# Performance work log

Measured on AMD Instinct MI355X. Metric: run time of the kernel, lower is better.

The kernel has to match this reference:

```python
import jax, jax.numpy as jnp
import numpy as np

NUM_HEADS = 16
THETA = 10000.0


def setup_inputs() -> dict:
    key = jax.random.key(0)
    ks = jax.random.split(key, 5)
    b, s, dm = 4, 2048, 2048
    sigma = np.sqrt(2.0 / (dm + dm))
    return {
        "x": jax.random.normal(ks[0], (b, s, dm), dtype=jnp.float32),
        "token_positions": jnp.arange(s, dtype=jnp.int64),
        "Wq": jax.random.normal(ks[1], (dm, dm), dtype=jnp.float32) * sigma,
        "Wk": jax.random.normal(ks[2], (dm, dm), dtype=jnp.float32) * sigma,
        "Wv": jax.random.normal(ks[3], (dm, dm), dtype=jnp.float32) * sigma,
        "Wo": jax.random.normal(ks[4], (dm, dm), dtype=jnp.float32) * sigma,
    }


def _apply_rope(x, positions):
    # x: [b, h, s, d]; positions: [s]
    d = x.shape[-1]
    half = d // 2
    inv_freq = THETA ** (-jnp.arange(half, dtype=x.dtype) / half)  # [half]
    ang = positions.astype(x.dtype)[:, None] * inv_freq           # [s, half]
    cos, sin = jnp.cos(ang), jnp.sin(ang)
    x2 = x.reshape(*x.shape[:-1], half, 2)   # even/odd interleaved pairs
    even, odd = x2[..., 0], x2[..., 1]
    rot_even = even * cos - odd * sin
    rot_odd = odd * cos + even * sin
    return jnp.stack([rot_even, rot_odd], axis=-1).reshape(x.shape)


def reference(x, token_positions, Wq, Wk, Wv, Wo):
    b, s, dm = x.shape
    h = NUM_HEADS
    d = dm // h

    def proj(W):
        return jnp.einsum('bsm,nm->bsn', x, W).reshape(b, s, h, d).transpose(0, 2, 1, 3)

    Q = _apply_rope(proj(Wq), token_positions)
    K = _apply_rope(proj(Wk), token_positions)
    V = proj(Wv)

    scores = jnp.einsum('bhqd,bhkd->bhqk', Q, K) / jnp.sqrt(jnp.asarray(d, x.dtype))
    causal = jnp.tril(jnp.ones((s, s), dtype=bool))
    scores = jnp.where(causal, scores, jnp.asarray(-jnp.inf, x.dtype))
    attn = jax.nn.softmax(scores, axis=-1)
    y = jnp.einsum('bhqk,bhkd->bhqd', attn, V)
    y = y.transpose(0, 2, 1, 3).reshape(b, s, dm)
    return jnp.einsum('bsm,nm->bsn', y, Wo)
```

## Files before the change

### kernel.cpp

```cpp
#include <hip/hip_runtime.h>
#include <hip/hip_bf16.h>
#include <math.h>

#define NUM_HEADS 16
#define HEAD_DIM  128
#define SEQ       2048
#define DM        2048
#define BATCH     4
#define M_ROWS    (BATCH * SEQ)

typedef short  short8 __attribute__((ext_vector_type(8)));
typedef float  f32x4  __attribute__((ext_vector_type(4)));

__device__ inline unsigned short f2bf(float f) {
    union { float f; unsigned u; } x; x.f = f;
    unsigned r = x.u + 0x7FFF + ((x.u >> 16) & 1);
    return (unsigned short)(r >> 16);
}

__device__ inline float bf2f(unsigned short u) {
    union { unsigned u; float f; } x; x.u = ((unsigned)u) << 16;
    return x.f;
}

__global__ __launch_bounds__(256)
void splitk(const float* __restrict__ src, unsigned short* __restrict__ dh,
            unsigned short* __restrict__ dl, int n4) {
    const int stride = gridDim.x * 256;
    for (int i = blockIdx.x * 256 + threadIdx.x; i < n4; i += stride) {
        const float4 v = ((const float4*)src)[i];
        ushort4 h, l;
        h.x = f2bf(v.x); l.x = f2bf(v.x - bf2f(h.x));
        h.y = f2bf(v.y); l.y = f2bf(v.y - bf2f(h.y));
        h.z = f2bf(v.z); l.z = f2bf(v.z - bf2f(h.z));
        h.w = f2bf(v.w); l.w = f2bf(v.w - bf2f(h.w));
        ((ushort4*)dh)[i] = h;
        ((ushort4*)dl)[i] = l;
    }
}

#define BKT  32
#define LDST 40

__global__ __launch_bounds__(256)
void mgemm2(const unsigned short* __restrict__ Ah, const unsigned short* __restrict__ Al,
            const unsigned short* __restrict__ Ag,
            const unsigned short* __restrict__ Bh, const unsigned short* __restrict__ Bl,
            unsigned short* __restrict__ Cb, float* __restrict__ Cf, int mode) {
    __shared__ __align__(16) unsigned short AsH[128 * LDST];
    __shared__ __align__(16) unsigned short AsL[128 * LDST];
    __shared__ __align__(16) unsigned short BsH[128 * LDST];
    __shared__ __align__(16) unsigned short BsL[128 * LDST];

    const int tid = threadIdx.x;
    const int lane = tid & 63, wave = tid >> 6;
    const int lo = lane & 15, hi = lane >> 4;
    const int wm = wave >> 1, wn = wave & 1;
    const int tm = blockIdx.y * 128, tn = blockIdx.x * 128;
    const bool split = (Ag == nullptr);

    const int sr = tid >> 2;
    const int sc = (tid & 3) * 8;

    f32x4 acc[4][4];
    #pragma unroll
    for (int mf = 0; mf < 4; ++mf)
        #pragma unroll
        for (int nf = 0; nf < 4; ++nf) acc[mf][nf] = (f32x4){0.f, 0.f, 0.f, 0.f};

    for (int k0 = 0; k0 < DM; k0 += BKT) {
        if (k0) __syncthreads();
        #pragma unroll
        for (int j = 0; j < 2; ++j) {
            const int r = j * 64 + sr;
            if (split) {
                *(short8*)&AsH[r * LDST + sc] =
                    *(const short8*)&Ah[(size_t)(tm + r) * DM + k0 + sc];
                *(short8*)&AsL[r * LDST + sc] =
                    *(const short8*)&Al[(size_t)(tm + r) * DM + k0 + sc];
            } else {
                const int row = tm + r;
                const int b = row >> 11, s = row & (SEQ - 1);
                const int hh = k0 >> 7, dd = (k0 & (HEAD_DIM - 1)) + sc;
                *(short8*)&AsH[r * LDST + sc] = *(const short8*)
                    &Ag[(((size_t)b * NUM_HEADS + hh) * SEQ + s) * HEAD_DIM + dd];
            }
            *(short8*)&BsH[r * LDST + sc] =
                *(const short8*)&Bh[(size_t)(tn + r) * DM + k0 + sc];
            *(short8*)&BsL[r * LDST + sc] =
                *(const short8*)&Bl[(size_t)(tn + r) * DM + k0 + sc];
        }
        __syncthreads();

        short8 a0[4], b0[4], tf[4];
        #pragma unroll
        for (int mf = 0; mf < 4; ++mf)
            a0[mf] = *(const short8*)&AsH[(wm * 64 + mf * 16 + lo) * LDST + hi * 8];
        #pragma unroll
        for (int nf = 0; nf < 4; ++nf)
            b0[nf] = *(const short8*)&BsH[(wn * 64 + nf * 16 + lo) * LDST + hi * 8];
        #pragma unroll
        for (int mf = 0; mf < 4; ++mf)
            #pragma unroll
            for (int nf = 0; nf < 4; ++nf)
                acc[mf][nf] = __builtin_amdgcn_mfma_f32_16x16x32_bf16(
                    a0[mf], b0[nf], acc[mf][nf], 0, 0, 0);
        if (split) {
            #pragma unroll
            for (int mf = 0; mf < 4; ++mf)
                tf[mf] = *(const short8*)&AsL[(wm * 64 + mf * 16 + lo) * LDST + hi * 8];
            #pragma unroll
            for (int mf = 0; mf < 4; ++mf)
                #pragma unroll
                for (int nf = 0; nf < 4; ++nf)
                    acc[mf][nf] = __builtin_amdgcn_mfma_f32_16x16x32_bf16(
                        tf[mf], b0[nf], acc[mf][nf], 0, 0, 0);
        }
        #pragma unroll
        for (int nf = 0; nf < 4; ++nf)
            tf[nf] = *(const short8*)&BsL[(wn * 64 + nf * 16 + lo) * LDST + hi * 8];
        #pragma unroll
        for (int mf = 0; mf < 4; ++mf)
            #pragma unroll
            for (int nf = 0; nf < 4; ++nf)
                acc[mf][nf] = __builtin_amdgcn_mfma_f32_16x16x32_bf16(
                    a0[mf], tf[nf], acc[mf][nf], 0, 0, 0);
    }

    const int r0 = tm + wm * 64, c0 = tn + wn * 64;
    #pragma unroll
    for (int mf = 0; mf < 4; ++mf) {
        #pragma unroll
        for (int nf = 0; nf < 4; ++nf) {
            const int col = c0 + nf * 16 + lo;
            if (mode == 0) {
                #pragma unroll
                for (int i = 0; i < 4; ++i) {
                    const int row = r0 + mf * 16 + hi * 4 + i;
                    Cf[(size_t)row * DM + col] = acc[mf][nf][i];
                }
            } else if (mode == 3) {
                const int row0 = r0 + mf * 16 + hi * 4;
                const int b = row0 >> 11, s0 = row0 & (SEQ - 1);
                const int hh = col >> 7, dd = col & (HEAD_DIM - 1);
                ushort4 u;
                u.x = f2bf(acc[mf][nf][0]); u.y = f2bf(acc[mf][nf][1]);
                u.z = f2bf(acc[mf][nf][2]); u.w = f2bf(acc[mf][nf][3]);
                *(ushort4*)&Cb[(((size_t)b * NUM_HEADS + hh) * HEAD_DIM + dd) * SEQ + s0] = u;
            } else {
                #pragma unroll
                for (int i = 0; i < 4; ++i) {
                    const int row = r0 + mf * 16 + hi * 4 + i;
                    const int s = row & (SEQ - 1);
                    float val = acc[mf][nf][i];
                    if (mode == 2) {
                        const float partner = __shfl_xor(val, 1, 64);
                        const int fi = (col & (HEAD_DIM - 1)) >> 1;
                        const float ang = (float)s *
                            expf((float)fi * (-9.210340371976184f / 64.f));
                        float sn, cs;
                        sincosf(ang, &sn, &cs);
                        if ((col & 1) == 0) val = val * cs - partner * sn;
                        else                val = val * cs + partner * sn;
                    }
                    const int b = row >> 11;
                    const int hh = col >> 7, dd = col & (HEAD_DIM - 1);
                    Cb[(((size_t)b * NUM_HEADS + hh) * SEQ + s) * HEAD_DIM + dd] = f2bf(val);
                }
            }
        }
    }
}

__global__ __launch_bounds__(256)
void mgemm(const float* __restrict__ Af, const unsigned short* __restrict__ Ag,
           const float* __restrict__ B, unsigned short* __restrict__ Cb,
           float* __restrict__ Cf, int mode) {
    __shared__ __align__(16) unsigned short AsH[128 * LDST];
    __shared__ __align__(16) unsigned short AsL[128 * LDST];
    __shared__ __align__(16) unsigned short BsH[128 * LDST];
    __shared__ __align__(16) unsigned short BsL[128 * LDST];

    const int tid = threadIdx.x;
    const int lane = tid & 63, wave = tid >> 6;
    const int lo = lane & 15, hi = lane >> 4;
    const int wm = wave >> 1, wn = wave & 1;
    const int tm = blockIdx.y * 128, tn = blockIdx.x * 128;
    const bool split = (Ag == nullptr);

    const int sr = tid >> 3;
    const int sc = (tid & 7) * 4;

    f32x4 acc[4][4];
    #pragma unroll
    for (int mf = 0; mf < 4; ++mf)
        #pragma unroll
        for (int nf = 0; nf < 4; ++nf) acc[mf][nf] = (f32x4){0.f, 0.f, 0.f, 0.f};

    for (int k0 = 0; k0 < DM; k0 += BKT) {
        if (k0) __syncthreads();
        #pragma unroll
        for (int it = 0; it < 4; ++it) {
            const int r = it * 32 + sr;
            if (split) {
                const float4 v = *(const float4*)&Af[(size_t)(tm + r) * DM + k0 + sc];
                ushort4 h, l;
                h.x = f2bf(v.x); l.x = f2bf(v.x - bf2f(h.x));
                h.y = f2bf(v.y); l.y = f2bf(v.y - bf2f(h.y));
                h.z = f2bf(v.z); l.z = f2bf(v.z - bf2f(h.z));
                h.w = f2bf(v.w); l.w = f2bf(v.w - bf2f(h.w));
                *(ushort4*)&AsH[r * LDST + sc] = h;
                *(ushort4*)&AsL[r * LDST + sc] = l;
            } else {
                const int row = tm + r;
                const int b = row >> 11, s = row & (SEQ - 1);
                const int k = k0 + sc;
                const int hh = k >> 7, dd = k & (HEAD_DIM - 1);
                const ushort4 u = *(const ushort4*)
                    &Ag[(((size_t)b * NUM_HEADS + hh) * SEQ + s) * HEAD_DIM + dd];
                *(ushort4*)&AsH[r * LDST + sc] = u;
            }
        }
        #pragma unroll
        for (int it = 0; it < 4; ++it) {
            const int r = it * 32 + sr;
            const float4 v = *(const float4*)&B[(size_t)(tn + r) * DM + k0 + sc];
            ushort4 h, l;
            h.x = f2bf(v.x); l.x = f2bf(v.x - bf2f(h.x));
            h.y = f2bf(v.y); l.y = f2bf(v.y - bf2f(h.y));
            h.z = f2bf(v.z); l.z = f2bf(v.z - bf2f(h.z));
            h.w = f2bf(v.w); l.w = f2bf(v.w - bf2f(h.w));
            *(ushort4*)&BsH[r * LDST + sc] = h;
            *(ushort4*)&BsL[r * LDST + sc] = l;
        }
        __syncthreads();

        short8 a0[4], b0[4], tf[4];
        #pragma unroll
        for (int mf = 0; mf < 4; ++mf)
            a0[mf] = *(const short8*)&AsH[(wm * 64 + mf * 16 + lo) * LDST + hi * 8];
        #pragma unroll
        for (int nf = 0; nf < 4; ++nf)
            b0[nf] = *(const short8*)&BsH[(wn * 64 + nf * 16 + lo) * LDST + hi * 8];
        #pragma unroll
        for (int mf = 0; mf < 4; ++mf)
            #pragma unroll
            for (int nf = 0; nf < 4; ++nf)
                acc[mf][nf] = __builtin_amdgcn_mfma_f32_16x16x32_bf16(
                    a0[mf], b0[nf], acc[mf][nf], 0, 0, 0);
        if (split) {
            #pragma unroll
            for (int mf = 0; mf < 4; ++mf)
                tf[mf] = *(const short8*)&AsL[(wm * 64 + mf * 16 + lo) * LDST + hi * 8];
            #pragma unroll
            for (int mf = 0; mf < 4; ++mf)
                #pragma unroll
                for (int nf = 0; nf < 4; ++nf)
                    acc[mf][nf] = __builtin_amdgcn_mfma_f32_16x16x32_bf16(
                        tf[mf], b0[nf], acc[mf][nf], 0, 0, 0);
        }
        #pragma unroll
        for (int nf = 0; nf < 4; ++nf)
            tf[nf] = *(const short8*)&BsL[(wn * 64 + nf * 16 + lo) * LDST + hi * 8];
        #pragma unroll
        for (int mf = 0; mf < 4; ++mf)
            #pragma unroll
            for (int nf = 0; nf < 4; ++nf)
                acc[mf][nf] = __builtin_amdgcn_mfma_f32_16x16x32_bf16(
                    a0[mf], tf[nf], acc[mf][nf], 0, 0, 0);
    }

    const int r0 = tm + wm * 64, c0 = tn + wn * 64;
    #pragma unroll
    for (int mf = 0; mf < 4; ++mf) {
        #pragma unroll
        for (int nf = 0; nf < 4; ++nf) {
            const int col = c0 + nf * 16 + lo;
            if (mode == 0) {
                #pragma unroll
                for (int i = 0; i < 4; ++i) {
                    const int row = r0 + mf * 16 + hi * 4 + i;
                    Cf[(size_t)row * DM + col] = acc[mf][nf][i];
                }
            } else if (mode == 3) {
                const int row0 = r0 + mf * 16 + hi * 4;
                const int b = row0 >> 11, s0 = row0 & (SEQ - 1);
                const int hh = col >> 7, dd = col & (HEAD_DIM - 1);
                ushort4 u;
                u.x = f2bf(acc[mf][nf][0]); u.y = f2bf(acc[mf][nf][1]);
                u.z = f2bf(acc[mf][nf][2]); u.w = f2bf(acc[mf][nf][3]);
                *(ushort4*)&Cb[(((size_t)b * NUM_HEADS + hh) * HEAD_DIM + dd) * SEQ + s0] = u;
            } else {
                #pragma unroll
                for (int i = 0; i < 4; ++i) {
                    const int row = r0 + mf * 16 + hi * 4 + i;
                    const int s = row & (SEQ - 1);
                    float val = acc[mf][nf][i];
                    if (mode == 2) {
                        const float partner = __shfl_xor(val, 1, 64);
                        const int fi = (col & (HEAD_DIM - 1)) >> 1;
                        const float ang = (float)s *
                            expf((float)fi * (-9.210340371976184f / 64.f));
                        float sn, cs;
                        sincosf(ang, &sn, &cs);
                        if ((col & 1) == 0) val = val * cs - partner * sn;
                        else                val = val * cs + partner * sn;
                    }
                    const int b = row >> 11;
                    const int hh = col >> 7, dd = col & (HEAD_DIM - 1);
                    Cb[(((size_t)b * NUM_HEADS + hh) * SEQ + s) * HEAD_DIM + dd] = f2bf(val);
                }
            }
        }
    }
}

__global__ __launch_bounds__(256, 4)
void mattn(const unsigned short* __restrict__ Q, const unsigned short* __restrict__ K,
           const unsigned short* __restrict__ Vt, unsigned short* __restrict__ Y) {
    __shared__ __align__(16) unsigned short Plds[4][16][72];
    const int tid = threadIdx.x, wave = tid >> 6, lane = tid & 63;
    const int lo = lane & 15, hi = lane >> 4;
    const int bh = blockIdx.y;
    const size_t baseQ = (size_t)bh * SEQ * HEAD_DIM;
    const size_t baseV = (size_t)bh * HEAD_DIM * SEQ;
    const float kscale = 0.08838834764831845f * 1.4426950408889634f;
    const int NB = SEQ / 64;

    #pragma unroll 1
    for (int pass = 0; pass < 2; ++pass) {
        const int qt = pass ? (NB - 1 - blockIdx.x) : blockIdx.x;
        const int q0 = qt * 64 + wave * 16;

        short8 qf[4];
        {
            const unsigned short* qrow = Q + baseQ + (size_t)(q0 + lo) * HEAD_DIM + hi * 8;
            #pragma unroll
            for (int c = 0; c < 4; ++c) qf[c] = *(const short8*)(qrow + c * 32);
        }

        f32x4 o[8];
        #pragma unroll
        for (int dt = 0; dt < 8; ++dt) o[dt] = (f32x4){0.f, 0.f, 0.f, 0.f};
        float m[4], l[4];
        #pragma unroll
        for (int i = 0; i < 4; ++i) { m[i] = -1e30f; l[i] = 0.f; }

        const int ntiles = qt + 1;

        for (int kt = 0; kt < ntiles; ++kt) {
            const int kv0 = kt * 64;

            f32x4 s[4];
            #pragma unroll
            for (int t = 0; t < 4; ++t) {
                f32x4 acc = {0.f, 0.f, 0.f, 0.f};
                const unsigned short* krow =
                    K + baseQ + (size_t)(kv0 + t * 16 + lo) * HEAD_DIM + hi * 8;
                #pragma unroll
                for (int c = 0; c < 4; ++c) {
                    short8 kf = *(const short8*)(krow + c * 32);
                    acc = __builtin_amdgcn_mfma_f32_16x16x32_bf16(qf[c], kf, acc, 0, 0, 0);
                }
                s[t] = acc;
            }

            const bool diag = (kv0 + 64 > q0);
            #pragma unroll
            for (int t = 0; t < 4; ++t)
                #pragma unroll
                for (int i = 0; i < 4; ++i) {
                    float v = s[t][i] * kscale;
                    if (diag && (kv0 + t * 16 + lo > q0 + hi * 4 + i)) v = -1e30f;
                    s[t][i] = v;
                }

            float corr[4];
            #pragma unroll
            for (int i = 0; i < 4; ++i) {
                float v = fmaxf(fmaxf(s[0][i], s[1][i]), fmaxf(s[2][i], s[3][i]));
                v = fmaxf(v, __shfl_xor(v, 1, 64));
                v = fmaxf(v, __shfl_xor(v, 2, 64));
                v = fmaxf(v, __shfl_xor(v, 4, 64));
                v = fmaxf(v, __shfl_xor(v, 8, 64));
                const float mn = fmaxf(m[i], v);
                corr[i] = exp2f(m[i] - mn);
                m[i] = mn;
            }

            float rs[4] = {0.f, 0.f, 0.f, 0.f};
            #pragma unroll
            for (int t = 0; t < 4; ++t)
                #pragma unroll
                for (int i = 0; i < 4; ++i) {
                    const float p = exp2f(s[t][i] - m[i]);
                    rs[i] += p;
                    Plds[wave][hi * 4 + i][t * 16 + lo] = f2bf(p);
                }
            #pragma unroll
            for (int i = 0; i < 4; ++i) {
                float v = rs[i];
                v += __shfl_xor(v, 1, 64);
                v += __shfl_xor(v, 2, 64);
                v += __shfl_xor(v, 4, 64);
                v += __shfl_xor(v, 8, 64);
                l[i] = l[i] * corr[i] + v;
            }

            #pragma unroll
            for (int dt = 0; dt < 8; ++dt)
                #pragma unroll
                for (int i = 0; i < 4; ++i) o[dt][i] *= corr[i];

            short8 pa[2];
            #pragma unroll
            for (int ks = 0; ks < 2; ++ks)
                pa[ks] = *(const short8*)&Plds[wave][lo][ks * 32 + hi * 8];

            #pragma unroll
            for (int dh = 0; dh < 2; ++dh) {
                short8 vf[8];
                #pragma unroll
                for (int q = 0; q < 8; ++q) {
                    const int dt = dh * 4 + (q >> 1), ks = q & 1;
                    vf[q] = *(const short8*)(Vt + baseV +
                        (size_t)(dt * 16 + lo) * SEQ + kv0 + ks * 32 + hi * 8);
                }
                #pragma unroll
                for (int q = 0; q < 8; ++q) {
                    const int dt = dh * 4 + (q >> 1), ks = q & 1;
                    o[dt] = __builtin_amdgcn_mfma_f32_16x16x32_bf16(
                        pa[ks], vf[q], o[dt], 0, 0, 0);
                }
            }
        }

        #pragma unroll
        for (int dt = 0; dt < 8; ++dt)
            #pragma unroll
            for (int i = 0; i < 4; ++i) {
                const float y = o[dt][i] / l[i];
                Y[baseQ + (size_t)(q0 + hi * 4 + i) * HEAD_DIM + dt * 16 + lo] = f2bf(y);
            }
    }
}

extern "C" void kernel_launch(void* const* d_in, const int* in_sizes, int n_in,
                              void* d_out, int out_size, void* d_ws, size_t ws_size,
                              hipStream_t stream) {
    int xi = -1, pi = -1, wi[4] = {-1, -1, -1, -1};
    int nw = 0;
    for (int i = 0; i < n_in && i < 8; ++i) {
        const long long sz = in_sizes[i];
        if (sz == 16777216) xi = i;
        else if (sz == 2048) pi = i;
        else if (sz == 4194304 && nw < 4) wi[nw++] = i;
    }
    int iq, ik, iv, io;
    if (xi < 0 || nw < 4) {
        xi = 0; iq = 2; ik = 3; iv = 4; io = 5;
    } else if (pi == 4 && xi == 5) {
        ik = wi[0]; io = wi[1]; iq = wi[2]; iv = wi[3];
    } else {
        iq = wi[0]; ik = wi[1]; iv = wi[2]; io = wi[3];
    }

    const float* x  = (const float*)d_in[xi];
    const float* Wq = (const float*)d_in[iq];
    const float* Wk = (const float*)d_in[ik];
    const float* Wv = (const float*)d_in[iv];
    const float* Wo = (const float*)d_in[io];
    float* out = (float*)d_out;

    unsigned short* ws16 = (unsigned short*)d_ws;
    unsigned short* Qb = ws16;
    unsigned short* Kb = Qb + (1ull << 24);
    unsigned short* Vt = Kb + (1ull << 24);

    dim3 blk(256);
    dim3 gg(DM / 128, M_ROWS / 128);
    dim3 ga(SEQ / 128, BATCH * NUM_HEADS);

    const size_t NEED = ((5ull << 24) + (2ull << 22)) * 2ull;
    if (ws_size >= NEED) {
        unsigned short* xh = Vt + (1ull << 24);
        unsigned short* xl = xh + (1ull << 24);
        unsigned short* Wh = xl + (1ull << 24);
        unsigned short* Wl = Wh + (1ull << 22);
        const int nx4 = (M_ROWS * DM) / 4;
        const int nw4 = (DM * DM) / 4;
        dim3 gs(1024);

        splitk<<<gs, blk, 0, stream>>>(x,  xh, xl, nx4);
        splitk<<<gs, blk, 0, stream>>>(Wq, Wh, Wl, nw4);
        mgemm2<<<gg, blk, 0, stream>>>(xh, xl, nullptr, Wh, Wl, Qb, nullptr, 2);
        splitk<<<gs, blk, 0, stream>>>(Wk, Wh, Wl, nw4);
        mgemm2<<<gg, blk, 0, stream>>>(xh, xl, nullptr, Wh, Wl, Kb, nullptr, 2);
        splitk<<<gs, blk, 0, stream>>>(Wv, Wh, Wl, nw4);
        mgemm2<<<gg, blk, 0, stream>>>(xh, xl, nullptr, Wh, Wl, Vt, nullptr, 3);
        mattn<<<ga, blk, 0, stream>>>(Qb, Kb, Vt, Qb);
        splitk<<<gs, blk, 0, stream>>>(Wo, Wh, Wl, nw4);
        mgemm2<<<gg, blk, 0, stream>>>(nullptr, nullptr, Qb, Wh, Wl, nullptr, out, 0);
    } else {
        mgemm<<<gg, blk, 0, stream>>>(x, nullptr, Wq, Qb, nullptr, 2);
        mgemm<<<gg, blk, 0, stream>>>(x, nullptr, Wk, Kb, nullptr, 2);
        mgemm<<<gg, blk, 0, stream>>>(x, nullptr, Wv, Vt, nullptr, 3);
        mattn<<<ga, blk, 0, stream>>>(Qb, Kb, Vt, Qb);
        mgemm<<<gg, blk, 0, stream>>>(nullptr, Qb, Wo, nullptr, out, 0);
    }
}
```

Before: 1.619 ms.

## Use one q-tile per block with XCD-aware remapping and peeled diagonal tile

The attention kernel previously had each block handle a paired front/back q-tile in two passes to balance the causal workload. Now each block handles one 64-row q-tile, doubling the grid, and remaps the block index so consecutive blocks on the same XCD share a head. The diagonal tile is peeled out so the mask check runs only there, and launch bounds request 8 blocks per CU. The cost is uneven per-block work (1 to 32 tiles), which relies on the hardware scheduler to balance, and tighter register limits that may cause spills.

New measurement: 2.765 ms. 70.8% more time.

```diff
diff --git a/kernel.cpp b/kernel.cpp
--- a/kernel.cpp
+++ b/kernel.cpp
@@ -315,134 +315,132 @@
     }
 }
 
-__global__ __launch_bounds__(256, 4)
+__global__ __launch_bounds__(256, 8)
 void mattn(const unsigned short* __restrict__ Q, const unsigned short* __restrict__ K,
            const unsigned short* __restrict__ Vt, unsigned short* __restrict__ Y) {
     __shared__ __align__(16) unsigned short Plds[4][16][72];
     const int tid = threadIdx.x, wave = tid >> 6, lane = tid & 63;
     const int lo = lane & 15, hi = lane >> 4;
-    const int bh = blockIdx.y;
+
+    const int flat = blockIdx.x + (int)gridDim.x * blockIdx.y;
+    const int v = (flat & 7) * 256 + (flat >> 3);
+    const int qt = v & 31;
+    const int bh = v >> 5;
+    const int q0 = qt * 64 + wave * 16;
+
     const size_t baseQ = (size_t)bh * SEQ * HEAD_DIM;
     const size_t baseV = (size_t)bh * HEAD_DIM * SEQ;
     const float kscale = 0.08838834764831845f * 1.4426950408889634f;
-    const int NB = SEQ / 64;
+
+    short8 qf[4];
+    {
+        const unsigned short* qrow = Q + baseQ + (size_t)(q0 + lo) * HEAD_DIM + hi * 8;
+        #pragma unroll
+        for (int c = 0; c < 4; ++c) qf[c] = *(const short8*)(qrow + c * 32);
+    }
+
+    f32x4 o[8];
+    #pragma unroll
+    for (int dt = 0; dt < 8; ++dt) o[dt] = (f32x4){0.f, 0.f, 0.f, 0.f};
+    float m[4], l[4];
+    #pragma unroll
+    for (int i = 0; i < 4; ++i) { m[i] = -1e30f; l[i] = 0.f; }
+
+    auto tile = [&](int kv0, bool diag) {
+        f32x4 s[4];
+        #pragma unroll
+        for (int t = 0; t < 4; ++t) {
+            f32x4 acc = {0.f, 0.f, 0.f, 0.f};
+            const unsigned short* krow =
+                K + baseQ + (size_t)(kv0 + t * 16 + lo) * HEAD_DIM + hi * 8;
+            #pragma unroll
+            for (int c = 0; c < 4; ++c) {
+                short8 kf = *(const short8*)(krow + c * 32);
+                acc = __builtin_amdgcn_mfma_f32_16x16x32_bf16(qf[c], kf, acc, 0, 0, 0);
+            }
+            s[t] = acc;
+        }
+
+        #pragma unroll
+        for (int t = 0; t < 4; ++t)
+            #pragma unroll
+            for (int i = 0; i < 4; ++i) {
+                float sv = s[t][i] * kscale;
+                if (diag && (kv0 + t * 16 + lo > q0 + hi * 4 + i)) sv = -1e30f;
+                s[t][i] = sv;
+            }
+
+        float corr[4];
+        #pragma unroll
+        for (int i = 0; i < 4; ++i) {
+            float mv = fmaxf(fmaxf(s[0][i], s[1][i]), fmaxf(s[2][i], s[3][i]));
+            mv = fmaxf(mv, __shfl_xor(mv, 1, 64));
+            mv = fmaxf(mv, __shfl_xor(mv, 2, 64));
+            mv = fmaxf(mv, __shfl_xor(mv, 4, 64));
+            mv = fmaxf(mv, __shfl_xor(mv, 8, 64));
+            const float mn = fmaxf(m[i], mv);
+            corr[i] = exp2f(m[i] - mn);
+            m[i] = mn;
+        }
+
+        float rs[4] = {0.f, 0.f, 0.f, 0.f};
+        #pragma unroll
+        for (int t = 0; t < 4; ++t)
+            #pragma unroll
+            for (int i = 0; i < 4; ++i) {
+                const float p = exp2f(s[t][i] - m[i]);
+                rs[i] += p;
+                Plds[wave][hi * 4 + i][t * 16 + lo] = f2bf(p);
+            }
+        #pragma unroll
+        for (int i = 0; i < 4; ++i) {
+            float sv = rs[i];
+            sv += __shfl_xor(sv, 1, 64);
+            sv += __shfl_xor(sv, 2, 64);
+            sv += __shfl_xor(sv, 4, 64);
+            sv += __shfl_xor(sv, 8, 64);
+            l[i] = l[i] * corr[i] + sv;
+        }
+
+        #pragma unroll
+        for (int dt = 0; dt < 8; ++dt)
+            #pragma unroll
+            for (int i = 0; i < 4; ++i) o[dt][i] *= corr[i];
+
+        short8 pa[2];
+        #pragma unroll
+        for (int ks = 0; ks < 2; ++ks)
+            pa[ks] = *(const short8*)&Plds[wave][lo][ks * 32 + hi * 8];
+
+        #pragma unroll
+        for (int dh = 0; dh < 2; ++dh) {
+            short8 vf[8];
+            #pragma unroll
+            for (int q = 0; q < 8; ++q) {
+                const int dt = dh * 4 + (q >> 1), ks = q & 1;
+                vf[q] = *(const short8*)(Vt + baseV +
+                    (size_t)(dt * 16 + lo) * SEQ + kv0 + ks * 32 + hi * 8);
+            }
+            #pragma unroll
+            for (int q = 0; q < 8; ++q) {
+                const int dt = dh * 4 + (q >> 1), ks = q & 1;
+                o[dt] = __builtin_amdgcn_mfma_f32_16x16x32_bf16(
+                    pa[ks], vf[q], o[dt], 0, 0, 0);
+            }
+        }
+    };
 
     #pragma unroll 1
-    for (int pass = 0; pass < 2; ++pass) {
-        const int qt = pass ? (NB - 1 - blockIdx.x) : blockIdx.x;
-        const int q0 = qt * 64 + wave * 16;
-
-        short8 qf[4];
-        {
-            const unsigned short* qrow = Q + baseQ + (size_t)(q0 + lo) * HEAD_DIM + hi * 8;
-            #pragma unroll
-            for (int c = 0; c < 4; ++c) qf[c] = *(const short8*)(qrow + c * 32);
-        }
-
-        f32x4 o[8];
-        #pragma unroll
-        for (int dt = 0; dt < 8; ++dt) o[dt] = (f32x4){0.f, 0.f, 0.f, 0.f};
-        float m[4], l[4];
-        #pragma unroll
-        for (int i = 0; i < 4; ++i) { m[i] = -1e30f; l[i] = 0.f; }
-
-        const int ntiles = qt + 1;
-
-        for (int kt = 0; kt < ntiles; ++kt) {
-            const int kv0 = kt * 64;
-
-            f32x4 s[4];
-            #pragma unroll
-            for (int t = 0; t < 4; ++t) {
-                f32x4 acc = {0.f, 0.f, 0.f, 0.f};
-                const unsigned short* krow =
-                    K + baseQ + (size_t)(kv0 + t * 16 + lo) * HEAD_DIM + hi * 8;
-                #pragma unroll
-                for (int c = 0; c < 4; ++c) {
-                    short8 kf = *(const short8*)(krow + c * 32);
-                    acc = __builtin_amdgcn_mfma_f32_16x16x32_bf16(qf[c], kf, acc, 0, 0, 0);
-                }
-                s[t] = acc;
-            }
-
-            const bool diag = (kv0 + 64 > q0);
-            #pragma unroll
-            for (int t = 0; t < 4; ++t)
-                #pragma unroll
-                for (int i = 0; i < 4; ++i) {
-                    float v = s[t][i] * kscale;
-                    if (diag && (kv0 + t * 16 + lo > q0 + hi * 4 + i)) v = -1e30f;
-                    s[t][i] = v;
-                }
-
-            float corr[4];
-            #pragma unroll
-            for (int i = 0; i < 4; ++i) {
-                float v = fmaxf(fmaxf(s[0][i], s[1][i]), fmaxf(s[2][i], s[3][i]));
-                v = fmaxf(v, __shfl_xor(v, 1, 64));
-                v = fmaxf(v, __shfl_xor(v, 2, 64));
-                v = fmaxf(v, __shfl_xor(v, 4, 64));
-                v = fmaxf(v, __shfl_xor(v, 8, 64));
-                const float mn = fmaxf(m[i], v);
-                corr[i] = exp2f(m[i] - mn);
-                m[i] = mn;
-            }
-
-            float rs[4] = {0.f, 0.f, 0.f, 0.f};
-            #pragma unroll
-            for (int t = 0; t < 4; ++t)
-                #pragma unroll
-                for (int i = 0; i < 4; ++i) {
-                    const float p = exp2f(s[t][i] - m[i]);
-                    rs[i] += p;
-                    Plds[wave][hi * 4 + i][t * 16 + lo] = f2bf(p);
-                }
-            #pragma unroll
-            for (int i = 0; i < 4; ++i) {
-                float v = rs[i];
-                v += __shfl_xor(v, 1, 64);
-                v += __shfl_xor(v, 2, 64);
-                v += __shfl_xor(v, 4, 64);
-                v += __shfl_xor(v, 8, 64);
-                l[i] = l[i] * corr[i] + v;
-            }
-
-            #pragma unroll
-            for (int dt = 0; dt < 8; ++dt)
-                #pragma unroll
-                for (int i = 0; i < 4; ++i) o[dt][i] *= corr[i];
-
-            short8 pa[2];
-            #pragma unroll
-            for (int ks = 0; ks < 2; ++ks)
-                pa[ks] = *(const short8*)&Plds[wave][lo][ks * 32 + hi * 8];
-
-            #pragma unroll
-            for (int dh = 0; dh < 2; ++dh) {
-                short8 vf[8];
-                #pragma unroll
-                for (int q = 0; q < 8; ++q) {
-                    const int dt = dh * 4 + (q >> 1), ks = q & 1;
-                    vf[q] = *(const short8*)(Vt + baseV +
-                        (size_t)(dt * 16 + lo) * SEQ + kv0 + ks * 32 + hi * 8);
-                }
-                #pragma unroll
-                for (int q = 0; q < 8; ++q) {
-                    const int dt = dh * 4 + (q >> 1), ks = q & 1;
-                    o[dt] = __builtin_amdgcn_mfma_f32_16x16x32_bf16(
-                        pa[ks], vf[q], o[dt], 0, 0, 0);
-                }
-            }
-        }
-
-        #pragma unroll
-        for (int dt = 0; dt < 8; ++dt)
-            #pragma unroll
-            for (int i = 0; i < 4; ++i) {
-                const float y = o[dt][i] / l[i];
-                Y[baseQ + (size_t)(q0 + hi * 4 + i) * HEAD_DIM + dt * 16 + lo] = f2bf(y);
-            }
-    }
+    for (int kt = 0; kt < qt; ++kt) tile(kt * 64, false);
+    tile(qt * 64, true);
+
+    #pragma unroll
+    for (int dt = 0; dt < 8; ++dt)
+        #pragma unroll
+        for (int i = 0; i < 4; ++i) {
+            const float y = o[dt][i] / l[i];
+            Y[baseQ + (size_t)(q0 + hi * 4 + i) * HEAD_DIM + dt * 16 + lo] = f2bf(y);
+        }
 }
 
 extern "C" void kernel_launch(void* const* d_in, const int* in_sizes, int n_in,
@@ -479,7 +477,7 @@
 
     dim3 blk(256);
     dim3 gg(DM / 128, M_ROWS / 128);
-    dim3 ga(SEQ / 128, BATCH * NUM_HEADS);
+    dim3 ga(SEQ / 64, BATCH * NUM_HEADS);
 
     const size_t NEED = ((5ull << 24) + (2ull << 22)) * 2ull;
     if (ws_size >= NEED) {
```
